# Kernel optimization log

Hardware: AMD Instinct MI355X
Metric: run time of the kernel (lower is better)

## Reference

```python
import jax, jax.numpy as jnp
import numpy as np

N = 30000      # nodes
E = 300000     # edges (before self-loops)
F_NODE = 32; F_EDGE = 16
HID = 64       # hidden_channels
H = 4; C = 64  # heads, per-head channels (GATConv out_channels = HID)
NEG_SLOPE_ATT = 0.2   # GATConv negative_slope
NEG_SLOPE_ACT = 0.01  # F.leaky_relu default
LN_EPS = 1e-5


def setup_inputs() -> dict:
    key = jax.random.key(0)
    ks = jax.random.split(key, 32)
    def w(k, shape, fan_in):
        return jax.random.normal(k, shape, jnp.float32) * (1.0 / np.sqrt(fan_in))
    inp = {
        "x": jax.random.normal(ks[0], (N, F_NODE), jnp.float32),
        "edge_index": jax.random.randint(ks[1], (2, E), 0, N),
        "edge_attr": jax.random.normal(ks[2], (E, F_EDGE), jnp.float32),
        "wn": w(ks[3], (F_NODE, HID), F_NODE), "bn": jnp.zeros((HID,), jnp.float32),
        "we": w(ks[4], (F_EDGE, HID), F_EDGE), "be": jnp.zeros((HID,), jnp.float32),
    }
    for i, off in ((1, 5), (2, 13)):
        inp[f"lin{i}"] = w(ks[off], (HID, H * C), HID)        # GATConv.lin
        inp[f"line{i}"] = w(ks[off + 1], (HID, H * C), HID)    # GATConv.lin_edge
        inp[f"as{i}"] = w(ks[off + 2], (H, C), C)              # att_src
        inp[f"ad{i}"] = w(ks[off + 3], (H, C), C)              # att_dst
        inp[f"ae{i}"] = w(ks[off + 4], (H, C), C)              # att_edge
        inp[f"b{i}"] = jnp.zeros((C,), jnp.float32)            # GATConv bias (concat=False -> C)
        inp[f"g{i}"] = jnp.ones((HID,), jnp.float32)           # LayerNorm weight
        inp[f"bt{i}"] = jnp.zeros((HID,), jnp.float32)         # LayerNorm bias
    return inp


def layernorm(x, g, b):
    mu = x.mean(-1, keepdims=True)
    v = ((x - mu) ** 2).mean(-1, keepdims=True)
    return (x - mu) / jnp.sqrt(v + LN_EPS) * g + b


def gat_layer(x, src, dst, e_attr, lin_w, lin_e_w, att_src, att_dst, att_edge, bias, n):
    # x: [n, HID]; e_attr: [E2, HID]; edge lists already include self-loops
    E2 = src.shape[0]
    h = (x @ lin_w).reshape(n, H, C)          # [n,H,C]
    e = (e_attr @ lin_e_w).reshape(E2, H, C)  # [E2,H,C]
    a_src = (h * att_src[None]).sum(-1)       # [n,H]
    a_dst = (h * att_dst[None]).sum(-1)       # [n,H]
    a_edge = (e * att_edge[None]).sum(-1)     # [E2,H]
    a = jax.nn.leaky_relu(a_src[src] + a_dst[dst] + a_edge, NEG_SLOPE_ATT)
    # scatter-softmax over destination neighborhoods (every node has a self-loop)
    m = jax.ops.segment_max(a, dst, num_segments=n)
    ex = jnp.exp(a - m[dst])
    den = jax.ops.segment_sum(ex, dst, num_segments=n)
    alpha = ex / den[dst]                     # [E2,H]
    out = jax.ops.segment_sum(h[src] * alpha[..., None], dst, num_segments=n)  # [n,H,C]
    return out.mean(axis=1) + bias, alpha     # concat=False: average heads


def reference(x, edge_index, edge_attr, wn, bn, we, be,
              lin1, line1, as1, ad1, ae1, b1, g1, bt1,
              lin2, line2, as2, ad2, ae2, b2, g2, bt2):
    n = x.shape[0]
    x = jax.nn.relu(x @ wn + bn)
    ea = jax.nn.relu(edge_attr @ we + be)
    src, dst = edge_index[0], edge_index[1]
    # PyG add_self_loops(fill_value='mean'): self-loop edge_attr = mean of incoming edge_attr
    ones = jnp.ones((src.shape[0],), ea.dtype)
    deg = jax.ops.segment_sum(ones, dst, num_segments=n)
    mean_ea = jax.ops.segment_sum(ea, dst, num_segments=n) / jnp.maximum(deg, 1.0)[:, None]
    loop = jnp.arange(n, dtype=src.dtype)
    src_f = jnp.concatenate([src, loop])
    dst_f = jnp.concatenate([dst, loop])
    ea_f = jnp.concatenate([ea, mean_ea], axis=0)
    h1, alpha1 = gat_layer(x, src_f, dst_f, ea_f, lin1, line1, as1, ad1, ae1, b1, n)
    h1 = layernorm(jax.nn.leaky_relu(h1, NEG_SLOPE_ACT), g1, bt1)
    # dropout is identity in eval mode
    h2, alpha2 = gat_layer(h1, src_f, dst_f, ea_f, lin2, line2, as2, ad2, ae2, b2, n)
    h2 = layernorm(jax.nn.leaky_relu(h2, NEG_SLOPE_ACT), g2, bt2)
    return h2, alpha1, alpha2
```

## Files before the change

kernel.cpp:

```cpp
#include <hip/hip_runtime.h>

#define FN 32
#define FE 16
#define HID 64
#define HEADS 4
#define CHC 64

typedef float f32x4 __attribute__((ext_vector_type(4)));

__device__ __forceinline__ float bf2f(unsigned short u) {
  unsigned int x = ((unsigned int)u) << 16;
  return __builtin_bit_cast(float, x);
}
__device__ __forceinline__ unsigned short f2bf(float f) {
  unsigned int x = __builtin_bit_cast(unsigned int, f);
  unsigned int r = (x + 0x7fff + ((x >> 16) & 1)) >> 16;
  return (unsigned short)r;
}

__device__ __forceinline__ void reduce8_store(const float p[8],
    float* __restrict__ arr1, float* __restrict__ arr2, size_t pos, int lane,
    float scale)
{
  float q[4];
  {
    bool hi = lane & 1;
    #pragma unroll
    for (int m = 0; m < 4; m++) {
      float keep = hi ? p[m + 4] : p[m];
      float send = hi ? p[m] : p[m + 4];
      q[m] = keep + __shfl_xor(send, 1);
    }
  }
  float r[2];
  {
    bool hi = lane & 2;
    #pragma unroll
    for (int m = 0; m < 2; m++) {
      float keep = hi ? q[m + 2] : q[m];
      float send = hi ? q[m] : q[m + 2];
      r[m] = keep + __shfl_xor(send, 2);
    }
  }
  float s;
  {
    bool hi = lane & 4;
    float keep = hi ? r[1] : r[0];
    float send = hi ? r[0] : r[1];
    s = keep + __shfl_xor(send, 4);
  }
  s += __shfl_xor(s, 8);
  s += __shfl_xor(s, 16);
  s += __shfl_xor(s, 32);
  if (lane < 8) {
    int entry = ((lane & 1) << 2) | (lane & 2) | ((lane >> 2) & 1);
    if (entry < 4) arr1[pos * 4 + entry] = s * scale;
    else           arr2[pos * 4 + entry - 4] = s * scale;
  }
}

__global__ __launch_bounds__(256) void k_vecs(
    const float* __restrict__ lin1, const float* __restrict__ line1,
    const float* __restrict__ as1, const float* __restrict__ ad1,
    const float* __restrict__ ae1,
    const float* __restrict__ lin2, const float* __restrict__ line2,
    const float* __restrict__ as2, const float* __restrict__ ad2,
    const float* __restrict__ ae2,
    float* __restrict__ vS, float* __restrict__ vD, float* __restrict__ vE)
{
  int bi = blockIdx.x;
  int l = bi / 3, kind = bi % 3;
  const float* lin = (kind == 2) ? (l ? line2 : line1) : (l ? lin2 : lin1);
  const float* att = (kind == 0) ? (l ? as2 : as1)
                   : (kind == 1) ? (l ? ad2 : ad1) : (l ? ae2 : ae1);
  float* out = ((kind == 0) ? vS : (kind == 1) ? vD : vE) + l * 256;
  int t = threadIdx.x;
  int c = t >> 2, hd = t & 3;
  float acc = 0.f;
  for (int cc = 0; cc < CHC; cc++)
    acc += lin[c * (HEADS * CHC) + hd * CHC + cc] * att[hd * CHC + cc];
  out[c * 4 + hd] = acc;
}

__global__ __launch_bounds__(256) void k_x1(const float* __restrict__ x,
    const float* __restrict__ wn, const float* __restrict__ bn,
    const float* __restrict__ vS, const float* __restrict__ vD,
    float* __restrict__ x1, float* __restrict__ ssrc, float* __restrict__ sdst,
    int n)
{
  int t = threadIdx.x; int w = t >> 6; int lane = t & 63;
  int v = blockIdx.x * 4 + w;
  __shared__ float xs[4][FN];
  if (v < n && lane < FN) xs[w][lane] = x[(size_t)v * FN + lane];
  __syncthreads();
  if (v >= n) return;
  float acc = bn[lane];
  #pragma unroll
  for (int k = 0; k < FN; k++) acc += xs[w][k] * wn[k * HID + lane];
  acc = fmaxf(acc, 0.f);
  x1[(size_t)v * HID + lane] = acc;
  float4 s4 = ((const float4*)vS)[lane];
  float4 d4 = ((const float4*)vD)[lane];
  float p[8] = {acc * s4.x, acc * s4.y, acc * s4.z, acc * s4.w,
                acc * d4.x, acc * d4.y, acc * d4.z, acc * d4.w};
  reduce8_store(p, ssrc, sdst, (size_t)v, lane, 1.f);
}

__global__ __launch_bounds__(256) void k_deg(const int* __restrict__ dst,
                                             int* __restrict__ deg, int E)
{
  int e = blockIdx.x * 256 + threadIdx.x;
  if (e < E) atomicAdd(&deg[dst[e]], 1);
}

__global__ __launch_bounds__(1024) void k_scan1(const int* __restrict__ deg,
    int* __restrict__ rowptr, int* __restrict__ bsum, int n)
{
  __shared__ int wsum[16];
  int t = threadIdx.x, wv = t >> 6, lane = t & 63;
  int i = blockIdx.x * 1024 + t;
  int val = (i < n) ? deg[i] : 0;
  int sc = val;
  #pragma unroll
  for (int off = 1; off < 64; off <<= 1) {
    int u = __shfl_up(sc, off);
    if (lane >= off) sc += u;
  }
  if (lane == 63) wsum[wv] = sc;
  __syncthreads();
  int woff = 0;
  #pragma unroll
  for (int k = 0; k < 16; k++) woff += (k < wv) ? wsum[k] : 0;
  if (i < n) rowptr[i] = woff + sc - val;
  if (t == 0) {
    int tot = 0;
    #pragma unroll
    for (int k = 0; k < 16; k++) tot += wsum[k];
    bsum[blockIdx.x] = tot;
  }
}

__global__ __launch_bounds__(1024) void k_scan2(const int* __restrict__ bsum,
    int* __restrict__ boff, int* __restrict__ rowptr, int nb, int n)
{
  __shared__ int wsum[16];
  int t = threadIdx.x, wv = t >> 6, lane = t & 63;
  int val = (t < nb) ? bsum[t] : 0;
  int sc = val;
  #pragma unroll
  for (int off = 1; off < 64; off <<= 1) {
    int u = __shfl_up(sc, off);
    if (lane >= off) sc += u;
  }
  if (lane == 63) wsum[wv] = sc;
  __syncthreads();
  int woff = 0;
  #pragma unroll
  for (int k = 0; k < 16; k++) woff += (k < wv) ? wsum[k] : 0;
  if (t < nb) boff[t] = woff + sc - val;
  if (t == 0) {
    int tot = 0;
    #pragma unroll
    for (int k = 0; k < 16; k++) tot += wsum[k];
    rowptr[n] = tot;
  }
}

__global__ __launch_bounds__(1024) void k_scan3(int* __restrict__ rowptr,
    const int* __restrict__ boff, int n)
{
  int i = blockIdx.x * 1024 + threadIdx.x;
  if (i < n) rowptr[i] += boff[blockIdx.x];
}

__global__ __launch_bounds__(256) void k_fill(const int* __restrict__ src,
    const int* __restrict__ dst, const int* __restrict__ rowptr,
    int* __restrict__ cnt, int* __restrict__ eid, int* __restrict__ srcs,
    int* __restrict__ perm, int E)
{
  int e = blockIdx.x * 256 + threadIdx.x;
  if (e < E) {
    int d = dst[e];
    int pos = rowptr[d] + atomicAdd(&cnt[d], 1);
    eid[pos] = e;
    srcs[pos] = src[e];
    perm[e] = pos;
  }
}

__global__ __launch_bounds__(256) void k_aeg_e(const float* __restrict__ eattr,
    const float* __restrict__ we, const float* __restrict__ be,
    const float* __restrict__ vE, const int* __restrict__ perm,
    float* __restrict__ aeg1, float* __restrict__ aeg2, int E)
{
  __shared__ float4 we_t4[HID][4];
  __shared__ float4 vE_s[2][HID];
  __shared__ float  be_s[HID];
  int t = threadIdx.x;
  for (int i = t; i < FE * HID; i += 256) {
    int k = i >> 6, c = i & 63;
    ((float*)we_t4)[c * 16 + k] = we[i];
  }
  for (int i = t; i < 512; i += 256) ((float*)vE_s)[i] = vE[i];
  if (t < HID) be_s[t] = be[t];
  __syncthreads();

  int e = blockIdx.x * 256 + t;
  if (e >= E) return;
  const float4* er = (const float4*)(eattr + (size_t)e * FE);
  float4 A = er[0], B = er[1], C4 = er[2], D = er[3];
  float ta[FE] = {A.x, A.y, A.z, A.w, B.x, B.y, B.z, B.w,
                  C4.x, C4.y, C4.z, C4.w, D.x, D.y, D.z, D.w};
  float4 acc1 = make_float4(0.f, 0.f, 0.f, 0.f);
  float4 acc2 = make_float4(0.f, 0.f, 0.f, 0.f);
  #pragma unroll 4
  for (int c = 0; c < HID; c++) {
    float4 w0 = we_t4[c][0], w1 = we_t4[c][1], w2 = we_t4[c][2], w3 = we_t4[c][3];
    float ea = be_s[c];
    ea += ta[0] * w0.x + ta[1] * w0.y + ta[2] * w0.z + ta[3] * w0.w;
    ea += ta[4] * w1.x + ta[5] * w1.y + ta[6] * w1.z + ta[7] * w1.w;
    ea += ta[8] * w2.x + ta[9] * w2.y + ta[10] * w2.z + ta[11] * w2.w;
    ea += ta[12] * w3.x + ta[13] * w3.y + ta[14] * w3.z + ta[15] * w3.w;
    ea = fmaxf(ea, 0.f);
    float4 u1 = vE_s[0][c], u2 = vE_s[1][c];
    acc1.x += ea * u1.x; acc1.y += ea * u1.y; acc1.z += ea * u1.z; acc1.w += ea * u1.w;
    acc2.x += ea * u2.x; acc2.y += ea * u2.y; acc2.z += ea * u2.z; acc2.w += ea * u2.w;
  }
  int pos = perm[e];
  *(float4*)(aeg1 + (size_t)pos * 4) = acc1;
  *(float4*)(aeg2 + (size_t)pos * 4) = acc2;
}

__global__ __launch_bounds__(256) void k_self_aeg(const int* __restrict__ rowptr,
    float* __restrict__ aeg1, float* __restrict__ aeg2, int E, int n)
{
  int t = threadIdx.x;
  int v = blockIdx.x * 32 + (t >> 3);
  if (v >= n) return;
  int ent = t & 7;
  int h = ent & 3;
  const float* srcp = (ent < 4) ? aeg1 : aeg2;
  int r0 = rowptr[v], r1 = rowptr[v + 1];
  float s = 0.f;
  for (int j = r0; j < r1; j++) s += srcp[(size_t)j * 4 + h];
  float m = s / fmaxf((float)(r1 - r0), 1.f);
  if (ent < 4) aeg1[((size_t)E + v) * 4 + h] = m;
  else         aeg2[((size_t)E + v) * 4 + h] = m;
}

#define NPB 16
__global__ __launch_bounds__(256) void k_h(const float* __restrict__ xin,
    const float* __restrict__ lin, unsigned short* __restrict__ h_bf, int n)
{
  int t = threadIdx.x;
  int v0 = blockIdx.x * NPB;
  __shared__ float xs[NPB][HID];
  for (int i = t; i < NPB * HID; i += 256) {
    int vv = v0 + (i >> 6);
    xs[i >> 6][i & 63] = (vv < n) ? xin[(size_t)vv * HID + (i & 63)] : 0.f;
  }
  __syncthreads();
  float acc[NPB];
  #pragma unroll
  for (int i = 0; i < NPB; i++) acc[i] = 0.f;
  for (int k = 0; k < HID; k++) {
    float lv = lin[k * 256 + t];
    #pragma unroll
    for (int i = 0; i < NPB; i++) acc[i] += xs[i][k] * lv;
  }
  #pragma unroll
  for (int i = 0; i < NPB; i++) {
    int v = v0 + i;
    if (v < n) h_bf[(size_t)v * 256 + t] = f2bf(acc[i]);
  }
}

template<bool DOTS>
__global__ __launch_bounds__(256) void k_node(
    const unsigned short* __restrict__ h_bf, const float* __restrict__ ssrc,
    const float* __restrict__ sdst, const float* __restrict__ aegc,
    const int* __restrict__ rowptr, const int* __restrict__ eidArr,
    const int* __restrict__ srcs, const float* __restrict__ bias,
    const float* __restrict__ gamma, const float* __restrict__ beta,
    const float* __restrict__ vS2, const float* __restrict__ vD2,
    float* __restrict__ alpha_out, float* __restrict__ xout,
    float* __restrict__ ssrc_o, float* __restrict__ sdst_o, int n, int E)
{
  __shared__ float als[4][64][4];
  int t = threadIdx.x; int wv = t >> 6, lane = t & 63;
  int v = blockIdx.x * 4 + wv;
  if (v >= n) return;
  int r0 = rowptr[v], r1 = rowptr[v + 1];
  int deg = r1 - r0, ne = deg + 1;
  int coff = lane * 4;
  int hh = lane >> 4;
  float acc0 = 0.f, acc1 = 0.f, acc2 = 0.f, acc3 = 0.f;
  const float4* aeg4 = (const float4*)aegc;
  const float4* ss4p = (const float4*)ssrc;
  float4 sd4 = ((const float4*)sdst)[v];

  if (ne <= 64) {
    int s = v, eo = E + v;
    if (lane < deg) { s = srcs[r0 + lane]; eo = eidArr[r0 + lane]; }
    bool valid = (lane < ne);
    float a0 = -INFINITY, a1 = -INFINITY, a2 = -INFINITY, a3 = -INFINITY;
    if (valid) {
      float4 ae4 = aeg4[(lane < deg) ? (r0 + lane) : (E + v)];
      float4 ss4 = ss4p[s];
      a0 = ss4.x + sd4.x + ae4.x; a0 = (a0 > 0.f) ? a0 : 0.2f * a0;
      a1 = ss4.y + sd4.y + ae4.y; a1 = (a1 > 0.f) ? a1 : 0.2f * a1;
      a2 = ss4.z + sd4.z + ae4.z; a2 = (a2 > 0.f) ? a2 : 0.2f * a2;
      a3 = ss4.w + sd4.w + ae4.w; a3 = (a3 > 0.f) ? a3 : 0.2f * a3;
    }
    float m0, m1, m2, m3;
    {
      bool hi0 = lane & 1;
      float k0 = hi0 ? a2 : a0, s0 = hi0 ? a0 : a2;
      float k1 = hi0 ? a3 : a1, s1 = hi0 ? a1 : a3;
      float q0 = fmaxf(k0, __shfl_xor(s0, 1));
      float q1 = fmaxf(k1, __shfl_xor(s1, 1));
      bool hi1 = lane & 2;
      float k2 = hi1 ? q1 : q0, s2 = hi1 ? q0 : q1;
      float r = fmaxf(k2, __shfl_xor(s2, 2));
      r = fmaxf(r, __shfl_xor(r, 4));
      r = fmaxf(r, __shfl_xor(r, 8));
      r = fmaxf(r, __shfl_xor(r, 16));
      r = fmaxf(r, __shfl_xor(r, 32));
      m0 = __shfl(r, 0); m1 = __shfl(r, 2); m2 = __shfl(r, 1); m3 = __shfl(r, 3);
    }
    float e0 = __expf(a0 - m0), e1 = __expf(a1 - m1);
    float e2 = __expf(a2 - m2), e3 = __expf(a3 - m3);
    float d0, d1, d2, d3;
    {
      bool hi0 = lane & 1;
      float k0 = hi0 ? e2 : e0, s0 = hi0 ? e0 : e2;
      float k1 = hi0 ? e3 : e1, s1 = hi0 ? e1 : e3;
      float q0 = k0 + __shfl_xor(s0, 1);
      float q1 = k1 + __shfl_xor(s1, 1);
      bool hi1 = lane & 2;
      float k2 = hi1 ? q1 : q0, s2 = hi1 ? q0 : q1;
      float r = k2 + __shfl_xor(s2, 2);
      r += __shfl_xor(r, 4);
      r += __shfl_xor(r, 8);
      r += __shfl_xor(r, 16);
      r += __shfl_xor(r, 32);
      d0 = __shfl(r, 0); d1 = __shfl(r, 2); d2 = __shfl(r, 1); d3 = __shfl(r, 3);
    }
    float4 alf = make_float4(e0 / d0, e1 / d1, e2 / d2, e3 / d3);
    if (valid) {
      f32x4 alv = {alf.x, alf.y, alf.z, alf.w};
      __builtin_nontemporal_store(alv, (f32x4*)alpha_out + eo);
    }
    *(float4*)als[wv][lane] = alf;
    __builtin_amdgcn_wave_barrier();
    __builtin_amdgcn_sched_barrier(0);
    int jj = 0;
    for (; jj + 3 < ne; jj += 4) {
      int s0 = __shfl(s, jj), s1 = __shfl(s, jj + 1);
      int s2 = __shfl(s, jj + 2), s3 = __shfl(s, jj + 3);
      float al0 = als[wv][jj][hh],     al1 = als[wv][jj + 1][hh];
      float al2 = als[wv][jj + 2][hh], al3 = als[wv][jj + 3][hh];
      uint2 u0 = *(const uint2*)(h_bf + (size_t)s0 * 256 + coff);
      uint2 u1 = *(const uint2*)(h_bf + (size_t)s1 * 256 + coff);
      uint2 u2 = *(const uint2*)(h_bf + (size_t)s2 * 256 + coff);
      uint2 u3 = *(const uint2*)(h_bf + (size_t)s3 * 256 + coff);
      acc0 += al0 * bf2f((unsigned short)(u0.x & 0xffff))
            + al1 * bf2f((unsigned short)(u1.x & 0xffff))
            + al2 * bf2f((unsigned short)(u2.x & 0xffff))
            + al3 * bf2f((unsigned short)(u3.x & 0xffff));
      acc1 += al0 * bf2f((unsigned short)(u0.x >> 16))
            + al1 * bf2f((unsigned short)(u1.x >> 16))
            + al2 * bf2f((unsigned short)(u2.x >> 16))
            + al3 * bf2f((unsigned short)(u3.x >> 16));
      acc2 += al0 * bf2f((unsigned short)(u0.y & 0xffff))
            + al1 * bf2f((unsigned short)(u1.y & 0xffff))
            + al2 * bf2f((unsigned short)(u2.y & 0xffff))
            + al3 * bf2f((unsigned short)(u3.y & 0xffff));
      acc3 += al0 * bf2f((unsigned short)(u0.y >> 16))
            + al1 * bf2f((unsigned short)(u1.y >> 16))
            + al2 * bf2f((unsigned short)(u2.y >> 16))
            + al3 * bf2f((unsigned short)(u3.y >> 16));
    }
    for (; jj < ne; jj++) {
      int s0 = __shfl(s, jj);
      float al0 = als[wv][jj][hh];
      uint2 u0 = *(const uint2*)(h_bf + (size_t)s0 * 256 + coff);
      acc0 += al0 * bf2f((unsigned short)(u0.x & 0xffff));
      acc1 += al0 * bf2f((unsigned short)(u0.x >> 16));
      acc2 += al0 * bf2f((unsigned short)(u0.y & 0xffff));
      acc3 += al0 * bf2f((unsigned short)(u0.y >> 16));
    }
  } else {
    int j4 = lane >> 2, hb = lane & 3;
    float sd = sdst[v * 4 + hb];
    float m = -INFINITY;
    for (int jb = 0; jb < ne; jb += 16) {
      int jc = jb + j4;
      if (jc < ne) {
        int s2 = (jc < deg) ? srcs[r0 + jc] : v;
        float ae = (jc < deg) ? aegc[(size_t)(r0 + jc) * 4 + hb]
                              : aegc[((size_t)E + v) * 4 + hb];
        float a = ssrc[s2 * 4 + hb] + sd + ae;
        a = (a > 0.f) ? a : 0.2f * a;
        m = fmaxf(m, a);
      }
    }
    m = fmaxf(m, __shfl_xor(m, 4));
    m = fmaxf(m, __shfl_xor(m, 8));
    m = fmaxf(m, __shfl_xor(m, 16));
    m = fmaxf(m, __shfl_xor(m, 32));
    float den = 0.f;
    for (int jb = 0; jb < ne; jb += 16) {
      int jc = jb + j4;
      if (jc < ne) {
        int s2 = (jc < deg) ? srcs[r0 + jc] : v;
        float ae = (jc < deg) ? aegc[(size_t)(r0 + jc) * 4 + hb]
                              : aegc[((size_t)E + v) * 4 + hb];
        float a = ssrc[s2 * 4 + hb] + sd + ae;
        a = (a > 0.f) ? a : 0.2f * a;
        den += __expf(a - m);
      }
    }
    den += __shfl_xor(den, 4);
    den += __shfl_xor(den, 8);
    den += __shfl_xor(den, 16);
    den += __shfl_xor(den, 32);
    float rden = 1.f / den;
    for (int jb = 0; jb < ne; jb += 16) {
      int jc = jb + j4;
      if (jc < ne) {
        int s2 = (jc < deg) ? srcs[r0 + jc] : v;
        int eo = (jc < deg) ? eidArr[r0 + jc] : E + v;
        float ae = (jc < deg) ? aegc[(size_t)(r0 + jc) * 4 + hb]
                              : aegc[((size_t)E + v) * 4 + hb];
        float a = ssrc[s2 * 4 + hb] + sd + ae;
        a = (a > 0.f) ? a : 0.2f * a;
        alpha_out[(size_t)eo * 4 + hb] = __expf(a - m) * rden;
      }
    }
    float sdh = __shfl(sd, hh);
    float mh  = __shfl(m, hh);
    float rdh = __shfl(rden, hh);
    for (int jc = 0; jc < ne; jc++) {
      int s0 = (jc < deg) ? srcs[r0 + jc] : v;
      size_t ap = (jc < deg) ? (size_t)(r0 + jc) : (size_t)E + v;
      float a = ssrc[s0 * 4 + hh] + sdh + aegc[ap * 4 + hh];
      a = (a > 0.f) ? a : 0.2f * a;
      float al = __expf(a - mh) * rdh;
      uint2 u = *(const uint2*)(h_bf + (size_t)s0 * 256 + coff);
      acc0 += al * bf2f((unsigned short)(u.x & 0xffff));
      acc1 += al * bf2f((unsigned short)(u.x >> 16));
      acc2 += al * bf2f((unsigned short)(u.y & 0xffff));
      acc3 += al * bf2f((unsigned short)(u.y >> 16));
    }
  }

  acc0 += __shfl_xor(acc0, 16); acc0 += __shfl_xor(acc0, 32);
  acc1 += __shfl_xor(acc1, 16); acc1 += __shfl_xor(acc1, 32);
  acc2 += __shfl_xor(acc2, 16); acc2 += __shfl_xor(acc2, 32);
  acc3 += __shfl_xor(acc3, 16); acc3 += __shfl_xor(acc3, 32);

  int c16 = lane & 15;
  float4 b4 = ((const float4*)bias)[c16];
  float v0 = acc0 * 0.25f + b4.x;
  float v1 = acc1 * 0.25f + b4.y;
  float v2 = acc2 * 0.25f + b4.z;
  float v3 = acc3 * 0.25f + b4.w;
  v0 = (v0 > 0.f) ? v0 : 0.01f * v0;
  v1 = (v1 > 0.f) ? v1 : 0.01f * v1;
  v2 = (v2 > 0.f) ? v2 : 0.01f * v2;
  v3 = (v3 > 0.f) ? v3 : 0.01f * v3;
  float mu = v0 + v1 + v2 + v3;
  mu += __shfl_xor(mu, 1); mu += __shfl_xor(mu, 2);
  mu += __shfl_xor(mu, 4); mu += __shfl_xor(mu, 8);
  mu *= (1.f / 64.f);
  float d0 = v0 - mu, d1 = v1 - mu, d2 = v2 - mu, d3 = v3 - mu;
  float var = d0 * d0 + d1 * d1 + d2 * d2 + d3 * d3;
  var += __shfl_xor(var, 1); var += __shfl_xor(var, 2);
  var += __shfl_xor(var, 4); var += __shfl_xor(var, 8);
  var *= (1.f / 64.f);
  float rstd = rsqrtf(var + 1e-5f);
  float4 g4 = ((const float4*)gamma)[c16];
  float4 be4 = ((const float4*)beta)[c16];
  float y0 = d0 * rstd * g4.x + be4.x;
  float y1 = d1 * rstd * g4.y + be4.y;
  float y2 = d2 * rstd * g4.z + be4.z;
  float y3 = d3 * rstd * g4.w + be4.w;
  if (lane < 16) {
    float4 y = make_float4(y0, y1, y2, y3);
    *(float4*)(xout + (size_t)v * HID + lane * 4) = y;
  }
  if constexpr (DOTS) {
    int c0 = c16 * 4;
    float4 vs0 = ((const float4*)vS2)[c0],     vs1 = ((const float4*)vS2)[c0 + 1];
    float4 vs2 = ((const float4*)vS2)[c0 + 2], vs3 = ((const float4*)vS2)[c0 + 3];
    float4 vd0 = ((const float4*)vD2)[c0],     vd1 = ((const float4*)vD2)[c0 + 1];
    float4 vd2 = ((const float4*)vD2)[c0 + 2], vd3 = ((const float4*)vD2)[c0 + 3];
    float p[8];
    p[0] = y0 * vs0.x + y1 * vs1.x + y2 * vs2.x + y3 * vs3.x;
    p[1] = y0 * vs0.y + y1 * vs1.y + y2 * vs2.y + y3 * vs3.y;
    p[2] = y0 * vs0.z + y1 * vs1.z + y2 * vs2.z + y3 * vs3.z;
    p[3] = y0 * vs0.w + y1 * vs1.w + y2 * vs2.w + y3 * vs3.w;
    p[4] = y0 * vd0.x + y1 * vd1.x + y2 * vd2.x + y3 * vd3.x;
    p[5] = y0 * vd0.y + y1 * vd1.y + y2 * vd2.y + y3 * vd3.y;
    p[6] = y0 * vd0.z + y1 * vd1.z + y2 * vd2.z + y3 * vd3.z;
    p[7] = y0 * vd0.w + y1 * vd1.w + y2 * vd2.w + y3 * vd3.w;
    reduce8_store(p, ssrc_o, sdst_o, (size_t)v, lane, 0.25f);
  }
}

extern "C" void kernel_launch(void* const* d_in, const int* in_sizes, int n_in,
                              void* d_out, int out_size, void* d_ws, size_t ws_size,
                              hipStream_t stream)
{
  const float* x     = (const float*)d_in[0];
  const int*   eidx  = (const int*)d_in[1];
  const float* eattr = (const float*)d_in[2];
  const float* wn    = (const float*)d_in[3];
  const float* bn    = (const float*)d_in[4];
  const float* we    = (const float*)d_in[5];
  const float* be    = (const float*)d_in[6];
  const float* lin1  = (const float*)d_in[7];
  const float* line1 = (const float*)d_in[8];
  const float* as1   = (const float*)d_in[9];
  const float* ad1   = (const float*)d_in[10];
  const float* ae1   = (const float*)d_in[11];
  const float* b1    = (const float*)d_in[12];
  const float* g1    = (const float*)d_in[13];
  const float* bt1   = (const float*)d_in[14];
  const float* lin2  = (const float*)d_in[15];
  const float* line2 = (const float*)d_in[16];
  const float* as2   = (const float*)d_in[17];
  const float* ad2   = (const float*)d_in[18];
  const float* ae2   = (const float*)d_in[19];
  const float* b2    = (const float*)d_in[20];
  const float* g2    = (const float*)d_in[21];
  const float* bt2   = (const float*)d_in[22];

  int n = in_sizes[0] / FN;
  int E = in_sizes[1] / 2;
  const int* srcA = eidx;
  const int* dstA = eidx + E;

  float* out_h2 = (float*)d_out;
  float* alpha1 = out_h2 + (size_t)n * HID;
  float* alpha2 = alpha1 + (size_t)(E + n) * 4;

  char* ws = (char*)d_ws;
  size_t off = 0;
  auto alloc = [&](size_t bytes) -> char* {
    char* p = ws + off;
    off += (bytes + 255) & ~(size_t)255;
    return p;
  };
  unsigned short* h_bf = (unsigned short*)alloc((size_t)n * 256 * 2);
  float* x1      = (float*)alloc((size_t)n * HID * 4);
  float* h1      = (float*)alloc((size_t)n * HID * 4);
  float* aeg1c   = (float*)alloc((size_t)(E + n) * 4 * 4);
  float* aeg2c   = (float*)alloc((size_t)(E + n) * 4 * 4);
  float* ssrc1   = (float*)alloc((size_t)n * 4 * 4);
  float* sdst1   = (float*)alloc((size_t)n * 4 * 4);
  float* ssrc2   = (float*)alloc((size_t)n * 4 * 4);
  float* sdst2   = (float*)alloc((size_t)n * 4 * 4);
  float* vS      = (float*)alloc(512 * 4);
  float* vD      = (float*)alloc(512 * 4);
  float* vE      = (float*)alloc(512 * 4);
  int*   deg     = (int*)alloc((size_t)n * 4);
  int*   cnt     = (int*)alloc((size_t)n * 4);
  int*   rowptr  = (int*)alloc((size_t)(n + 1) * 4);
  int*   eid     = (int*)alloc((size_t)E * 4);
  int*   srcs    = (int*)alloc((size_t)E * 4);
  int*   perm    = (int*)alloc((size_t)E * 4);
  int*   bsum    = (int*)alloc(1024 * 4);
  int*   boff    = (int*)alloc(1024 * 4);

  hipMemsetAsync(deg, 0, (size_t)n * 4, stream);
  hipMemsetAsync(cnt, 0, (size_t)n * 4, stream);

  int nb = (n + 1023) / 1024;
  k_vecs<<<6, 256, 0, stream>>>(lin1, line1, as1, ad1, ae1,
                                lin2, line2, as2, ad2, ae2, vS, vD, vE);
  k_x1<<<(n + 3) / 4, 256, 0, stream>>>(x, wn, bn, vS, vD, x1, ssrc1, sdst1, n);
  k_deg<<<(E + 255) / 256, 256, 0, stream>>>(dstA, deg, E);
  k_scan1<<<nb, 1024, 0, stream>>>(deg, rowptr, bsum, n);
  k_scan2<<<1, 1024, 0, stream>>>(bsum, boff, rowptr, nb, n);
  k_scan3<<<nb, 1024, 0, stream>>>(rowptr, boff, n);
  k_fill<<<(E + 255) / 256, 256, 0, stream>>>(srcA, dstA, rowptr, cnt, eid, srcs, perm, E);
  k_aeg_e<<<(E + 255) / 256, 256, 0, stream>>>(eattr, we, be, vE, perm, aeg1c, aeg2c, E);
  k_self_aeg<<<(n + 31) / 32, 256, 0, stream>>>(rowptr, aeg1c, aeg2c, E, n);

  k_h<<<(n + NPB - 1) / NPB, 256, 0, stream>>>(x1, lin1, h_bf, n);
  k_node<true><<<(n + 3) / 4, 256, 0, stream>>>(h_bf, ssrc1, sdst1, aeg1c,
      rowptr, eid, srcs, b1, g1, bt1, vS + 256, vD + 256,
      alpha1, h1, ssrc2, sdst2, n, E);
  k_h<<<(n + NPB - 1) / NPB, 256, 0, stream>>>(h1, lin2, h_bf, n);
  k_node<false><<<(n + 3) / 4, 256, 0, stream>>>(h_bf, ssrc2, sdst2, aeg2c,
      rowptr, eid, srcs, b2, g2, bt2, nullptr, nullptr,
      alpha2, out_h2, nullptr, nullptr, n, E);
}
```

Measured before the change: 228.2 us.

## Register-tile k_h, merge scan kernels, unroll gather by eight via LDS indices

The node-projection kernel k_h now gives each thread a 4x4 register tile, using float4 loads of the weights and shared-memory inputs and packed bf16 stores, in place of one output column per thread across 16 nodes. The second and third prefix-scan kernels are merged into one, where each block sums the earlier block totals serially, removing a launch. In k_node's small-degree path, source indices and attention weights are staged in LDS in a head-major layout. The gather loop then processes eight neighbours per iteration with vector LDS reads, and padding lanes carry zero weight. This removes the scalar tail loop but issues extra wasted loads when degree is not a multiple of eight.

Measured after the change: 223.9 us. Within noise of the previous version (-1.9%).

```diff
diff --git a/kernel.cpp b/kernel.cpp
--- a/kernel.cpp
+++ b/kernel.cpp
@@ -16,6 +16,9 @@
   unsigned int x = __builtin_bit_cast(unsigned int, f);
   unsigned int r = (x + 0x7fff + ((x >> 16) & 1)) >> 16;
   return (unsigned short)r;
+}
+__device__ __forceinline__ unsigned int pack2bf(float a, float b) {
+  return (unsigned int)f2bf(a) | ((unsigned int)f2bf(b) << 16);
 }
 
 __device__ __forceinline__ void reduce8_store(const float p[8],
@@ -140,37 +143,20 @@
   }
 }
 
-__global__ __launch_bounds__(1024) void k_scan2(const int* __restrict__ bsum,
-    int* __restrict__ boff, int* __restrict__ rowptr, int nb, int n)
-{
-  __shared__ int wsum[16];
-  int t = threadIdx.x, wv = t >> 6, lane = t & 63;
-  int val = (t < nb) ? bsum[t] : 0;
-  int sc = val;
-  #pragma unroll
-  for (int off = 1; off < 64; off <<= 1) {
-    int u = __shfl_up(sc, off);
-    if (lane >= off) sc += u;
-  }
-  if (lane == 63) wsum[wv] = sc;
-  __syncthreads();
-  int woff = 0;
-  #pragma unroll
-  for (int k = 0; k < 16; k++) woff += (k < wv) ? wsum[k] : 0;
-  if (t < nb) boff[t] = woff + sc - val;
-  if (t == 0) {
+__global__ __launch_bounds__(1024) void k_scan23(const int* __restrict__ bsum,
+    int* __restrict__ rowptr, int nb, int n)
+{
+  int b = blockIdx.x;
+  int t = threadIdx.x;
+  int off = 0;
+  for (int j = 0; j < b; j++) off += bsum[j];
+  int i = b * 1024 + t;
+  if (i < n) rowptr[i] += off;
+  if (b == 0 && t == 0) {
     int tot = 0;
-    #pragma unroll
-    for (int k = 0; k < 16; k++) tot += wsum[k];
+    for (int j = 0; j < nb; j++) tot += bsum[j];
     rowptr[n] = tot;
   }
-}
-
-__global__ __launch_bounds__(1024) void k_scan3(int* __restrict__ rowptr,
-    const int* __restrict__ boff, int n)
-{
-  int i = blockIdx.x * 1024 + threadIdx.x;
-  if (i < n) rowptr[i] += boff[blockIdx.x];
 }
 
 __global__ __launch_bounds__(256) void k_fill(const int* __restrict__ src,
@@ -248,30 +234,53 @@
   else         aeg2[((size_t)E + v) * 4 + h] = m;
 }
 
-#define NPB 16
 __global__ __launch_bounds__(256) void k_h(const float* __restrict__ xin,
     const float* __restrict__ lin, unsigned short* __restrict__ h_bf, int n)
 {
-  int t = threadIdx.x;
-  int v0 = blockIdx.x * NPB;
-  __shared__ float xs[NPB][HID];
-  for (int i = t; i < NPB * HID; i += 256) {
-    int vv = v0 + (i >> 6);
-    xs[i >> 6][i & 63] = (vv < n) ? xin[(size_t)vv * HID + (i & 63)] : 0.f;
+  int t = threadIdx.x, wv = t >> 6, lane = t & 63;
+  int v0 = blockIdx.x * 16;
+  __shared__ float xs[16][HID];
+  {
+    int node = t >> 4, ch4 = (t & 15) * 4;
+    int vv = v0 + node;
+    float4 val = make_float4(0.f, 0.f, 0.f, 0.f);
+    if (vv < n) val = *(const float4*)(xin + (size_t)vv * HID + ch4);
+    *(float4*)&xs[node][ch4] = val;
   }
   __syncthreads();
-  float acc[NPB];
+  float acc[4][4];
   #pragma unroll
-  for (int i = 0; i < NPB; i++) acc[i] = 0.f;
-  for (int k = 0; k < HID; k++) {
-    float lv = lin[k * 256 + t];
+  for (int i = 0; i < 4; i++)
     #pragma unroll
-    for (int i = 0; i < NPB; i++) acc[i] += xs[i][k] * lv;
+    for (int j = 0; j < 4; j++) acc[i][j] = 0.f;
+  const float4* lin4 = (const float4*)lin;
+  int nd0 = wv * 4;
+  #pragma unroll 4
+  for (int kb = 0; kb < 16; kb++) {
+    float4 xv[4];
+    #pragma unroll
+    for (int i = 0; i < 4; i++) xv[i] = *(const float4*)&xs[nd0 + i][kb * 4];
+    float4 lv0 = lin4[(kb * 4 + 0) * 64 + lane];
+    float4 lv1 = lin4[(kb * 4 + 1) * 64 + lane];
+    float4 lv2 = lin4[(kb * 4 + 2) * 64 + lane];
+    float4 lv3 = lin4[(kb * 4 + 3) * 64 + lane];
+    #pragma unroll
+    for (int i = 0; i < 4; i++) {
+      acc[i][0] += xv[i].x * lv0.x + xv[i].y * lv1.x + xv[i].z * lv2.x + xv[i].w * lv3.x;
+      acc[i][1] += xv[i].x * lv0.y + xv[i].y * lv1.y + xv[i].z * lv2.y + xv[i].w * lv3.y;
+      acc[i][2] += xv[i].x * lv0.z + xv[i].y * lv1.z + xv[i].z * lv2.z + xv[i].w * lv3.z;
+      acc[i][3] += xv[i].x * lv0.w + xv[i].y * lv1.w + xv[i].z * lv2.w + xv[i].w * lv3.w;
+    }
   }
   #pragma unroll
-  for (int i = 0; i < NPB; i++) {
-    int v = v0 + i;
-    if (v < n) h_bf[(size_t)v * 256 + t] = f2bf(acc[i]);
+  for (int i = 0; i < 4; i++) {
+    int v = v0 + nd0 + i;
+    if (v < n) {
+      uint2 u;
+      u.x = pack2bf(acc[i][0], acc[i][1]);
+      u.y = pack2bf(acc[i][2], acc[i][3]);
+      *(uint2*)(h_bf + (size_t)v * 256 + lane * 4) = u;
+    }
   }
 }
 
@@ -286,7 +295,8 @@
     float* __restrict__ alpha_out, float* __restrict__ xout,
     float* __restrict__ ssrc_o, float* __restrict__ sdst_o, int n, int E)
 {
-  __shared__ float als[4][64][4];
+  __shared__ float als[4][4][64];
+  __shared__ int   svec[4][64];
   int t = threadIdx.x; int wv = t >> 6, lane = t & 63;
   int v = blockIdx.x * 4 + wv;
   if (v >= n) return;
@@ -351,44 +361,60 @@
       f32x4 alv = {alf.x, alf.y, alf.z, alf.w};
       __builtin_nontemporal_store(alv, (f32x4*)alpha_out + eo);
     }
-    *(float4*)als[wv][lane] = alf;
+    als[wv][0][lane] = alf.x;
+    als[wv][1][lane] = alf.y;
+    als[wv][2][lane] = alf.z;
+    als[wv][3][lane] = alf.w;
+    svec[wv][lane] = s;
     __builtin_amdgcn_wave_barrier();
     __builtin_amdgcn_sched_barrier(0);
-    int jj = 0;
-    for (; jj + 3 < ne; jj += 4) {
-      int s0 = __shfl(s, jj), s1 = __shfl(s, jj + 1);
-      int s2 = __shfl(s, jj + 2), s3 = __shfl(s, jj + 3);
-      float al0 = als[wv][jj][hh],     al1 = als[wv][jj + 1][hh];
-      float al2 = als[wv][jj + 2][hh], al3 = als[wv][jj + 3][hh];
-      uint2 u0 = *(const uint2*)(h_bf + (size_t)s0 * 256 + coff);
-      uint2 u1 = *(const uint2*)(h_bf + (size_t)s1 * 256 + coff);
-      uint2 u2 = *(const uint2*)(h_bf + (size_t)s2 * 256 + coff);
-      uint2 u3 = *(const uint2*)(h_bf + (size_t)s3 * 256 + coff);
-      acc0 += al0 * bf2f((unsigned short)(u0.x & 0xffff))
-            + al1 * bf2f((unsigned short)(u1.x & 0xffff))
-            + al2 * bf2f((unsigned short)(u2.x & 0xffff))
-            + al3 * bf2f((unsigned short)(u3.x & 0xffff));
-      acc1 += al0 * bf2f((unsigned short)(u0.x >> 16))
-            + al1 * bf2f((unsigned short)(u1.x >> 16))
-            + al2 * bf2f((unsigned short)(u2.x >> 16))
-            + al3 * bf2f((unsigned short)(u3.x >> 16));
-      acc2 += al0 * bf2f((unsigned short)(u0.y & 0xffff))
-            + al1 * bf2f((unsigned short)(u1.y & 0xffff))
-            + al2 * bf2f((unsigned short)(u2.y & 0xffff))
-            + al3 * bf2f((unsigned short)(u3.y & 0xffff));
-      acc3 += al0 * bf2f((unsigned short)(u0.y >> 16))
-            + al1 * bf2f((unsigned short)(u1.y >> 16))
-            + al2 * bf2f((unsigned short)(u2.y >> 16))
-            + al3 * bf2f((unsigned short)(u3.y >> 16));
-    }
-    for (; jj < ne; jj++) {
-      int s0 = __shfl(s, jj);
-      float al0 = als[wv][jj][hh];
-      uint2 u0 = *(const uint2*)(h_bf + (size_t)s0 * 256 + coff);
-      acc0 += al0 * bf2f((unsigned short)(u0.x & 0xffff));
-      acc1 += al0 * bf2f((unsigned short)(u0.x >> 16));
-      acc2 += al0 * bf2f((unsigned short)(u0.y & 0xffff));
-      acc3 += al0 * bf2f((unsigned short)(u0.y >> 16));
+    const float* alsh = als[wv][hh];
+    const int* svp = svec[wv];
+    for (int jj = 0; jj < ne; jj += 8) {
+      int4 sv0 = *(const int4*)(svp + jj);
+      int4 sv1 = *(const int4*)(svp + jj + 4);
+      float4 al0 = *(const float4*)(alsh + jj);
+      float4 al1 = *(const float4*)(alsh + jj + 4);
+      uint2 u0 = *(const uint2*)(h_bf + (size_t)sv0.x * 256 + coff);
+      uint2 u1 = *(const uint2*)(h_bf + (size_t)sv0.y * 256 + coff);
+      uint2 u2 = *(const uint2*)(h_bf + (size_t)sv0.z * 256 + coff);
+      uint2 u3 = *(const uint2*)(h_bf + (size_t)sv0.w * 256 + coff);
+      uint2 u4 = *(const uint2*)(h_bf + (size_t)sv1.x * 256 + coff);
+      uint2 u5 = *(const uint2*)(h_bf + (size_t)sv1.y * 256 + coff);
+      uint2 u6 = *(const uint2*)(h_bf + (size_t)sv1.z * 256 + coff);
+      uint2 u7 = *(const uint2*)(h_bf + (size_t)sv1.w * 256 + coff);
+      acc0 += al0.x * bf2f((unsigned short)(u0.x & 0xffff))
+            + al0.y * bf2f((unsigned short)(u1.x & 0xffff))
+            + al0.z * bf2f((unsigned short)(u2.x & 0xffff))
+            + al0.w * bf2f((unsigned short)(u3.x & 0xffff))
+            + al1.x * bf2f((unsigned short)(u4.x & 0xffff))
+            + al1.y * bf2f((unsigned short)(u5.x & 0xffff))
+            + al1.z * bf2f((unsigned short)(u6.x & 0xffff))
+            + al1.w * bf2f((unsigned short)(u7.x & 0xffff));
+      acc1 += al0.x * bf2f((unsigned short)(u0.x >> 16))
+            + al0.y * bf2f((unsigned short)(u1.x >> 16))
+            + al0.z * bf2f((unsigned short)(u2.x >> 16))
+            + al0.w * bf2f((unsigned short)(u3.x >> 16))
+            + al1.x * bf2f((unsigned short)(u4.x >> 16))
+            + al1.y * bf2f((unsigned short)(u5.x >> 16))
+            + al1.z * bf2f((unsigned short)(u6.x >> 16))
+            + al1.w * bf2f((unsigned short)(u7.x >> 16));
+      acc2 += al0.x * bf2f((unsigned short)(u0.y & 0xffff))
+            + al0.y * bf2f((unsigned short)(u1.y & 0xffff))
+            + al0.z * bf2f((unsigned short)(u2.y & 0xffff))
+            + al0.w * bf2f((unsigned short)(u3.y & 0xffff))
+            + al1.x * bf2f((unsigned short)(u4.y & 0xffff))
+            + al1.y * bf2f((unsigned short)(u5.y & 0xffff))
+            + al1.z * bf2f((unsigned short)(u6.y & 0xffff))
+            + al1.w * bf2f((unsigned short)(u7.y & 0xffff));
+      acc3 += al0.x * bf2f((unsigned short)(u0.y >> 16))
+            + al0.y * bf2f((unsigned short)(u1.y >> 16))
+            + al0.z * bf2f((unsigned short)(u2.y >> 16))
+            + al0.w * bf2f((unsigned short)(u3.y >> 16))
+            + al1.x * bf2f((unsigned short)(u4.y >> 16))
+            + al1.y * bf2f((unsigned short)(u5.y >> 16))
+            + al1.z * bf2f((unsigned short)(u6.y >> 16))
+            + al1.w * bf2f((unsigned short)(u7.y >> 16));
     }
   } else {
     int j4 = lane >> 2, hb = lane & 3;
@@ -572,7 +598,6 @@
   int*   srcs    = (int*)alloc((size_t)E * 4);
   int*   perm    = (int*)alloc((size_t)E * 4);
   int*   bsum    = (int*)alloc(1024 * 4);
-  int*   boff    = (int*)alloc(1024 * 4);
 
   hipMemsetAsync(deg, 0, (size_t)n * 4, stream);
   hipMemsetAsync(cnt, 0, (size_t)n * 4, stream);
@@ -583,17 +608,16 @@
   k_x1<<<(n + 3) / 4, 256, 0, stream>>>(x, wn, bn, vS, vD, x1, ssrc1, sdst1, n);
   k_deg<<<(E + 255) / 256, 256, 0, stream>>>(dstA, deg, E);
   k_scan1<<<nb, 1024, 0, stream>>>(deg, rowptr, bsum, n);
-  k_scan2<<<1, 1024, 0, stream>>>(bsum, boff, rowptr, nb, n);
-  k_scan3<<<nb, 1024, 0, stream>>>(rowptr, boff, n);
+  k_scan23<<<nb, 1024, 0, stream>>>(bsum, rowptr, nb, n);
   k_fill<<<(E + 255) / 256, 256, 0, stream>>>(srcA, dstA, rowptr, cnt, eid, srcs, perm, E);
   k_aeg_e<<<(E + 255) / 256, 256, 0, stream>>>(eattr, we, be, vE, perm, aeg1c, aeg2c, E);
   k_self_aeg<<<(n + 31) / 32, 256, 0, stream>>>(rowptr, aeg1c, aeg2c, E, n);
 
-  k_h<<<(n + NPB - 1) / NPB, 256, 0, stream>>>(x1, lin1, h_bf, n);
+  k_h<<<(n + 15) / 16, 256, 0, stream>>>(x1, lin1, h_bf, n);
   k_node<true><<<(n + 3) / 4, 256, 0, stream>>>(h_bf, ssrc1, sdst1, aeg1c,
       rowptr, eid, srcs, b1, g1, bt1, vS + 256, vD + 256,
       alpha1, h1, ssrc2, sdst2, n, E);
-  k_h<<<(n + NPB - 1) / NPB, 256, 0, stream>>>(h1, lin2, h_bf, n);
+  k_h<<<(n + 15) / 16, 256, 0, stream>>>(h1, lin2, h_bf, n);
   k_node<false><<<(n + 3) / 4, 256, 0, stream>>>(h_bf, ssrc2, sdst2, aeg2c,
       rowptr, eid, srcs, b2, g2, bt2, nullptr, nullptr,
       alpha2, out_h2, nullptr, nullptr, n, E);
```
